# Optimization experiments

Measured on AMD Instinct MI355X. Metric: run time of the kernel, lower is better.

Reference implementation:

```python
import jax, jax.numpy as jnp
import numpy as np

B, S, D = 2, 2048, 1024
E, K = 8, 2
H = 1792  # round_up(int(1024*5/3)=1706, 256)


def setup_inputs() -> dict:
    key = jax.random.key(0)
    k1, k2, k3, k4, k5 = jax.random.split(key, 5)
    scale = 0.02
    x = jax.random.normal(k1, (B, S, D), dtype=jnp.float32)
    gate_w = jax.random.normal(k2, (E, D), dtype=jnp.float32) * scale   # nn.Linear(D,E).weight
    w_gate = jax.random.normal(k3, (E, D, H), dtype=jnp.float32) * scale
    w_up = jax.random.normal(k4, (E, D, H), dtype=jnp.float32) * scale
    w_down = jax.random.normal(k5, (E, H, D), dtype=jnp.float32) * scale
    return {"x": x, "gate_w": gate_w, "w_gate": w_gate, "w_up": w_up, "w_down": w_down}


def reference(x, gate_w, w_gate, w_up, w_down):
    b, s, d = x.shape
    x_flat = x.reshape(-1, d)                      # [T, D]
    # Gate computed in bf16 (torch autocast) then cast back to f32.
    logits = (x_flat.astype(jnp.bfloat16) @ gate_w.T.astype(jnp.bfloat16)).astype(jnp.float32)  # [T, E]
    topk_w, topk_idx = jax.lax.top_k(logits, K)    # [T, K]
    topk_w = jax.nn.softmax(topk_w, axis=-1)
    probs = jax.nn.softmax(logits, axis=-1)        # [T, E]
    mean_probs = probs.mean(0)                     # [E]
    load_balance_loss = E * jnp.sum(mean_probs ** 2)
    # Per-token combine weight for each expert (equivalent to sort/split/index_add combine).
    combine = jnp.sum(jax.nn.one_hot(topk_idx, E, dtype=x_flat.dtype) * topk_w[..., None], axis=1)  # [T, E]
    out = jnp.zeros_like(x_flat)
    for e in range(E):  # fixed small expert loop; math identical to grouped dispatch
        g = x_flat @ w_gate[e]                     # [T, H]
        u = x_flat @ w_up[e]                       # [T, H]
        y = (jax.nn.silu(g) * u) @ w_down[e]       # [T, D]
        out = out + y * combine[:, e:e + 1]
    return out.reshape(b, s, d), load_balance_loss, mean_probs
```

## Files before the change

kernel.cpp:

```cpp
#include <hip/hip_runtime.h>
#include <stdint.h>

#define TT 4096
#define DD 1024
#define EE 8
#define HH 1792
#define MP 10240
#define MT256 40
#define MT128 80

typedef __attribute__((ext_vector_type(8))) short short8;
typedef __attribute__((ext_vector_type(4))) short short4v;
typedef __attribute__((ext_vector_type(4))) float f32x4;

static __device__ __forceinline__ unsigned short f2bf(float f) {
  union { float f; uint32_t u; } v; v.f = f;
  return (unsigned short)((v.u + 0x7fffu + ((v.u >> 16) & 1u)) >> 16);
}
static __device__ __forceinline__ float bf2f(unsigned short h) {
  union { uint32_t u; float f; } v; v.u = ((uint32_t)h) << 16;
  return v.f;
}

static __device__ __forceinline__ void gll16(const void* g, const void* l) {
  __builtin_amdgcn_global_load_lds(
      (const __attribute__((address_space(1))) unsigned int*)g,
      (__attribute__((address_space(3))) unsigned int*)l, 16, 0, 0);
}

__global__ __launch_bounds__(256) void transpose_convert(
    const float* __restrict__ in, unsigned short* __restrict__ outp, int R, int C,
    int ilv, int sel) {
  __shared__ float t[64][68];
  const float* src = in + (size_t)blockIdx.z * R * C + (size_t)(blockIdx.x * 64) * C +
                     blockIdx.y * 64;
  unsigned short* dst = outp + (size_t)blockIdx.z * R * C * (ilv ? 2 : 1);
  const int tid = threadIdx.x;
  const int lr = tid >> 2, lc = (tid & 3) * 16;
#pragma unroll
  for (int q = 0; q < 4; ++q) {
    const f32x4 v = *(const f32x4*)(src + (size_t)lr * C + lc + 4 * q);
    t[lr][lc + 4 * q + 0] = v[0]; t[lr][lc + 4 * q + 1] = v[1];
    t[lr][lc + 4 * q + 2] = v[2]; t[lr][lc + 4 * q + 3] = v[3];
  }
  __syncthreads();
  unsigned short b[16];
#pragma unroll
  for (int q = 0; q < 16; ++q) b[q] = f2bf(t[lc + q][lr]);
  const int cg = blockIdx.y * 64 + lr;
  const int prow = ilv ? ((cg >> 4) * 32 + sel * 16 + (cg & 15)) : cg;
  unsigned short* d = dst + (size_t)prow * R + blockIdx.x * 64 + lc;
  *(short8*)(d) = *(const short8*)&b[0];
  *(short8*)(d + 8) = *(const short8*)&b[8];
}

__global__ __launch_bounds__(256) void gate_kernel(
    const float* __restrict__ x, const float* __restrict__ gw,
    float* __restrict__ combine, float* __restrict__ probs, int2* __restrict__ topk) {
  const int lane = threadIdx.x & 63;
  const int wave = threadIdx.x >> 6;
  const int t = blockIdx.x * 4 + wave;
  const float* xr = x + (size_t)t * DD;
  float acc[EE];
#pragma unroll
  for (int e = 0; e < EE; ++e) acc[e] = 0.f;
  for (int i = 0; i < DD / 64; ++i) {
    const int d = i * 64 + lane;
    const float xv = bf2f(f2bf(xr[d]));
#pragma unroll
    for (int e = 0; e < EE; ++e)
      acc[e] += xv * bf2f(f2bf(gw[e * DD + d]));
  }
#pragma unroll
  for (int e = 0; e < EE; ++e) {
#pragma unroll
    for (int off = 32; off > 0; off >>= 1)
      acc[e] += __shfl_xor(acc[e], off, 64);
  }
  if (lane == 0) {
    float lg[EE];
#pragma unroll
    for (int e = 0; e < EE; ++e) lg[e] = bf2f(f2bf(acc[e]));
    float m1 = -1e30f, m2 = -1e30f; int i1 = 0, i2 = 0;
#pragma unroll
    for (int e = 0; e < EE; ++e) {
      const float v = lg[e];
      if (v > m1) { m2 = m1; i2 = i1; m1 = v; i1 = e; }
      else if (v > m2) { m2 = v; i2 = e; }
    }
    const float e2 = expf(m2 - m1);
    const float w1 = 1.f / (1.f + e2);
    const float w2 = e2 * w1;
    float cb[EE];
#pragma unroll
    for (int e = 0; e < EE; ++e) cb[e] = 0.f;
    cb[i1] = w1; cb[i2] += w2;
    float p[EE]; float s = 0.f;
#pragma unroll
    for (int e = 0; e < EE; ++e) { p[e] = expf(lg[e] - m1); s += p[e]; }
    const float inv = 1.f / s;
#pragma unroll
    for (int e = 0; e < EE; ++e) {
      combine[(size_t)t * EE + e] = cb[e];
      probs[(size_t)t * EE + e] = p[e] * inv;
    }
    topk[t] = make_int2(i1, i2);
  }
}

__global__ __launch_bounds__(256) void reduce_kernel(
    const float* __restrict__ probs, float* __restrict__ tail) {
  const int tid = threadIdx.x;
  const int lane = tid & 63, wave = tid >> 6;
  float acc[EE];
#pragma unroll
  for (int e = 0; e < EE; ++e) acc[e] = 0.f;
  for (int t = tid; t < TT; t += 256) {
#pragma unroll
    for (int e = 0; e < EE; ++e) acc[e] += probs[(size_t)t * EE + e];
  }
#pragma unroll
  for (int e = 0; e < EE; ++e) {
#pragma unroll
    for (int off = 32; off > 0; off >>= 1)
      acc[e] += __shfl_xor(acc[e], off, 64);
  }
  __shared__ float sm[4][EE];
  if (lane == 0) {
#pragma unroll
    for (int e = 0; e < EE; ++e) sm[wave][e] = acc[e];
  }
  __syncthreads();
  if (tid == 0) {
    float loss = 0.f;
#pragma unroll
    for (int e = 0; e < EE; ++e) {
      const float m = (sm[0][e] + sm[1][e] + sm[2][e] + sm[3][e]) * (1.f / TT);
      tail[1 + e] = m;
      loss += m * m;
    }
    tail[0] = (float)EE * loss;
  }
}

__global__ __launch_bounds__(512) void route_kernel(
    const int2* __restrict__ topk, const float* __restrict__ combine,
    int* __restrict__ tok_list, float* __restrict__ wt_list,
    int* __restrict__ tab256, int* __restrict__ tab128) {
  const int lane = threadIdx.x & 63;
  const int e = threadIdx.x >> 6;
  __shared__ int cnts[EE], offs[EE];
  int cnt = 0;
  for (int i = 0; i < TT / 64; ++i) {
    const int2 k2 = topk[i * 64 + lane];
    cnt += __popcll(__ballot(k2.x == e || k2.y == e));
  }
  if (lane == 0) cnts[e] = cnt;
  __syncthreads();
  if (threadIdx.x == 0) {
    int off = 0, n256 = 0, n128 = 0;
    for (int f = 0; f < EE; ++f) {
      offs[f] = off;
      const int pc = (cnts[f] + 255) & ~255;
      for (int j = 0; j < (pc >> 8); ++j) {
        tab256[2 * n256] = f; tab256[2 * n256 + 1] = off + 256 * j; ++n256;
      }
      for (int j = 0; j < (pc >> 7); ++j) {
        tab128[2 * n128] = f; tab128[2 * n128 + 1] = off + 128 * j; ++n128;
      }
      off += pc;
    }
    for (; n256 < MT256; ++n256) { tab256[2 * n256] = -1; tab256[2 * n256 + 1] = 0; }
    for (; n128 < MT128; ++n128) { tab128[2 * n128] = -1; tab128[2 * n128 + 1] = 0; }
  }
  __syncthreads();
  int pos = offs[e];
  for (int i = 0; i < TT / 64; ++i) {
    const int t = i * 64 + lane;
    const int2 k2 = topk[t];
    const bool sel = (k2.x == e || k2.y == e);
    const unsigned long long m = __ballot(sel);
    if (sel) {
      const int p = pos + __popcll(m & ((1ull << lane) - 1ull));
      tok_list[p] = t;
      wt_list[p] = combine[(size_t)t * EE + e];
    }
    pos += __popcll(m);
  }
  const int pc = (cnt + 255) & ~255;
  for (int s = cnt + lane; s < pc; s += 64) {
    tok_list[offs[e] + s] = 0;
    wt_list[offs[e] + s] = 0.f;
  }
}

__global__ __launch_bounds__(256) void gather_x(
    const float* __restrict__ x, const int* __restrict__ tok_list,
    const int* __restrict__ tab256, unsigned short* __restrict__ xg) {
  const int e = tab256[2 * blockIdx.x];
  if (e < 0) return;
  const int row0 = tab256[2 * blockIdx.x + 1] + blockIdx.y * 16;
  const int tid = threadIdx.x;
#pragma unroll
  for (int i = 0; i < 16; ++i) {
    const int row = row0 + i;
    const int tok = tok_list[row];
    const f32x4 v = *(const f32x4*)(x + (size_t)tok * DD + tid * 4);
    unsigned short b[4] = {f2bf(v[0]), f2bf(v[1]), f2bf(v[2]), f2bf(v[3])};
    *(short4v*)(xg + (size_t)row * DD + tid * 4) = *(const short4v*)b;
  }
}

template <int MODE>
__global__ __launch_bounds__(256, 3) void gemm128(
    const unsigned short* __restrict__ Ab, const unsigned short* __restrict__ Bb,
    const int* __restrict__ tab, const int* __restrict__ tok_list,
    const float* __restrict__ wt_list, unsigned short* __restrict__ act,
    float* __restrict__ out) {
  constexpr int K   = (MODE == 0) ? DD : HH;
  constexpr int NBR = (MODE == 0) ? 2 * HH : DD;
  constexpr int NNT = NBR / 128;
  __shared__ unsigned short As[128 * 64];
  __shared__ unsigned short Bs[128 * 64];

  const int nwg = gridDim.x;
  const int wgid = (blockIdx.x & 7) * (nwg >> 3) + (blockIdx.x >> 3);
  const int mt = wgid / NNT, nt = wgid % NNT;
  const int e = tab[2 * mt];
  if (e < 0) return;
  const int row0 = tab[2 * mt + 1];
  const int n0 = nt * 128;

  const int tid = threadIdx.x, lane = tid & 63, wave = tid >> 6;
  const int wm = (wave >> 1) * 64, wn = (wave & 1) * 64;
  const int fr = lane & 15, hi = lane >> 4;

  const unsigned short* At = Ab + (size_t)row0 * K;
  const unsigned short* Bt = Bb + ((size_t)e * NBR + n0) * K;

  const int srel = tid * 16;
  const int srow0 = srel >> 7;
  const int sch = (srel >> 4) & 7;

  f32x4 acc[4][4];
#pragma unroll
  for (int i = 0; i < 4; ++i)
#pragma unroll
    for (int j = 0; j < 4; ++j) acc[i][j] = (f32x4){0.f, 0.f, 0.f, 0.f};

  for (int k0 = 0; k0 < K; k0 += 64) {
#pragma unroll
    for (int q = 0; q < 4; ++q) {
      const int row = q * 32 + srow0;
      gll16(At + (size_t)row * K + k0 + ((sch ^ (row & 7)) << 3),
            (const char*)As + q * 4096 + srel);
    }
#pragma unroll
    for (int q = 0; q < 4; ++q) {
      const int row = q * 32 + srow0;
      gll16(Bt + (size_t)row * K + k0 + ((sch ^ (row & 7)) << 3),
            (const char*)Bs + q * 4096 + srel);
    }
    __syncthreads();
#pragma unroll
    for (int kc = 0; kc < 2; ++kc) {
      short8 a[4], b[4];
#pragma unroll
      for (int i = 0; i < 4; ++i) {
        const int row = wm + i * 16 + fr;
        const int byt = (row * 128 + kc * 64 + hi * 16) ^ ((row & 7) << 4);
        a[i] = *(const short8*)((const char*)As + byt);
      }
#pragma unroll
      for (int j = 0; j < 4; ++j) {
        const int row = wn + j * 16 + fr;
        const int byt = (row * 128 + kc * 64 + hi * 16) ^ ((row & 7) << 4);
        b[j] = *(const short8*)((const char*)Bs + byt);
      }
#pragma unroll
      for (int i = 0; i < 4; ++i)
#pragma unroll
        for (int j = 0; j < 4; ++j)
          acc[i][j] = __builtin_amdgcn_mfma_f32_16x16x32_bf16(a[i], b[j], acc[i][j], 0, 0, 0);
    }
    __syncthreads();
  }

  const int r4 = hi * 4;
  if constexpr (MODE == 0) {
#pragma unroll
    for (int i = 0; i < 4; ++i)
#pragma unroll
      for (int r = 0; r < 4; ++r) {
        const int row = row0 + wm + i * 16 + r4 + r;
#pragma unroll
        for (int jj = 0; jj < 2; ++jj) {
          const float g = acc[i][2 * jj][r], u = acc[i][2 * jj + 1][r];
          const int nb = n0 + wn + jj * 32;
          const int h = ((nb >> 5) << 4) + fr;
          act[(size_t)row * HH + h] = f2bf((g / (1.f + expf(-g))) * u);
        }
      }
  } else {
#pragma unroll
    for (int i = 0; i < 4; ++i)
#pragma unroll
      for (int r = 0; r < 4; ++r) {
        const int rl = row0 + wm + i * 16 + r4 + r;
        const int tok = tok_list[rl];
        const float wt = wt_list[rl];
        if (wt != 0.f) {
#pragma unroll
          for (int j = 0; j < 4; ++j)
            unsafeAtomicAdd(&out[(size_t)tok * DD + n0 + wn + j * 16 + fr],
                            acc[i][j][r] * wt);
        }
      }
  }
}

extern "C" void kernel_launch(void* const* d_in, const int* in_sizes, int n_in,
                              void* d_out, int out_size, void* d_ws, size_t ws_size,
                              hipStream_t stream) {
  const float* x      = (const float*)d_in[0];
  const float* gw     = (const float*)d_in[1];
  const float* w_gate = (const float*)d_in[2];
  const float* w_up   = (const float*)d_in[3];
  const float* w_down = (const float*)d_in[4];
  float* out = (float*)d_out;
  float* tail = out + (size_t)TT * DD;

  char* w = (char*)d_ws;
  size_t o = 0;
  auto carve = [&](size_t bytes) { char* p = w + o; o += (bytes + 255) & ~255ull; return p; };
  unsigned short* wguT = (unsigned short*)carve((size_t)EE * 2 * HH * DD * 2);
  unsigned short* wdT  = (unsigned short*)carve((size_t)EE * DD * HH * 2);
  unsigned short* xg   = (unsigned short*)carve((size_t)MP * DD * 2);
  unsigned short* act  = (unsigned short*)carve((size_t)MP * HH * 2);
  float* combine = (float*)carve((size_t)TT * EE * 4);
  float* probs   = (float*)carve((size_t)TT * EE * 4);
  int2* topk     = (int2*)carve((size_t)TT * 8);
  int* tok_list  = (int*)carve((size_t)MP * 4);
  float* wt_list = (float*)carve((size_t)MP * 4);
  int* tab256    = (int*)carve((size_t)MT256 * 8);
  int* tab128    = (int*)carve((size_t)MT128 * 8);

  hipMemsetAsync(out, 0, (size_t)TT * DD * sizeof(float), stream);

  transpose_convert<<<dim3(DD / 64, HH / 64, EE), 256, 0, stream>>>(w_gate, wguT, DD, HH, 1, 0);
  transpose_convert<<<dim3(DD / 64, HH / 64, EE), 256, 0, stream>>>(w_up,   wguT, DD, HH, 1, 1);
  transpose_convert<<<dim3(HH / 64, DD / 64, EE), 256, 0, stream>>>(w_down, wdT,  HH, DD, 0, 0);

  gate_kernel<<<TT / 4, 256, 0, stream>>>(x, gw, combine, probs, topk);
  reduce_kernel<<<1, 256, 0, stream>>>(probs, tail);
  route_kernel<<<1, 512, 0, stream>>>(topk, combine, tok_list, wt_list, tab256, tab128);
  gather_x<<<dim3(MT256, 16), 256, 0, stream>>>(x, tok_list, tab256, xg);

  gemm128<0><<<MT128 * 28, 256, 0, stream>>>(xg, wguT, tab128, nullptr, nullptr, act, nullptr);
  gemm128<1><<<MT128 * 8, 256, 0, stream>>>(act, wdT, tab128, tok_list, wt_list, nullptr, out);
}
```

Baseline: 273.1 us.

## Replace gate/up GEMM with 256x256 double-buffered 8-wave pipelined kernel

```diff
diff --git a/kernel.cpp b/kernel.cpp
--- a/kernel.cpp
+++ b/kernel.cpp
@@ -211,15 +211,178 @@
   }
 }
 
-template <int MODE>
-__global__ __launch_bounds__(256, 3) void gemm128(
+#define MID_SYNC                                     \
+  __builtin_amdgcn_sched_barrier(0);                 \
+  __builtin_amdgcn_s_barrier();                      \
+  asm volatile("s_waitcnt lgkmcnt(0)" ::: "memory"); \
+  __builtin_amdgcn_sched_barrier(0);
+#define MID_SYNC_V4                                  \
+  __builtin_amdgcn_sched_barrier(0);                 \
+  asm volatile("s_waitcnt vmcnt(4)" ::: "memory");   \
+  __builtin_amdgcn_s_barrier();                      \
+  __builtin_amdgcn_sched_barrier(0);
+#define END_SYNC                                     \
+  __builtin_amdgcn_sched_barrier(0);                 \
+  __builtin_amdgcn_s_barrier();
+
+__global__ __launch_bounds__(512, 2) void gemm256(
+    const unsigned short* __restrict__ Ab, const unsigned short* __restrict__ Bb,
+    const int* __restrict__ tab, unsigned short* __restrict__ act) {
+  constexpr int K = DD;
+  constexpr int NK = K / 64;
+  constexpr int NNT = 14;
+  extern __shared__ char lds[];
+
+  const int nwg = gridDim.x;
+  const int wgid = (blockIdx.x & 7) * (nwg >> 3) + (blockIdx.x >> 3);
+  const int mt = wgid / NNT, nt = wgid % NNT;
+  const int e = tab[2 * mt];
+  if (e < 0) return;
+  const int row0 = tab[2 * mt + 1];
+  const int n0 = nt * 256;
+
+  const int tid = threadIdx.x, lane = tid & 63, wave = tid >> 6;
+  const int wm = (wave >> 2) * 128, wn = (wave & 3) * 64;
+  const int fr = lane & 15, hi = lane >> 4;
+
+  const unsigned short* At = Ab + (size_t)row0 * K;
+  const unsigned short* Bt = Bb + ((size_t)e * 2 * HH + n0) * K;
+
+  asm volatile("s_waitcnt vmcnt(0)" ::: "memory");
+
+  auto stage = [&](int u, int p, int h) {
+    const unsigned short* src = (h >= 2) ? Bt : At;
+    const int rbase = (h & 1) * 128;
+#pragma unroll
+    for (int q = 0; q < 2; ++q) {
+      const int rel = q * 8192 + tid * 16;
+      const int row = rel >> 7;
+      const int ch = (rel >> 4) & 7;
+      gll16(src + (size_t)(rbase + row) * K + u * 64 + ((ch ^ (row & 7)) << 3),
+            lds + p * 65536 + h * 16384 + rel);
+    }
+  };
+  auto rdA = [&](int p, int m, int kc) -> short8 {
+    const int lr = m & 127;
+    return *(const short8*)(lds + p * 65536 + ((m >> 7) << 14) + lr * 128 +
+                            ((((kc << 2) + hi) ^ (lr & 7)) << 4));
+  };
+  auto rdB = [&](int p, int n, int kc) -> short8 {
+    const int lr = n & 127;
+    return *(const short8*)(lds + p * 65536 + 32768 + ((n >> 7) << 14) + lr * 128 +
+                            ((((kc << 2) + hi) ^ (lr & 7)) << 4));
+  };
+
+  f32x4 acc[8][4];
+#pragma unroll
+  for (int i = 0; i < 8; ++i)
+#pragma unroll
+    for (int j = 0; j < 4; ++j) acc[i][j] = (f32x4){0.f, 0.f, 0.f, 0.f};
+  short8 a03[4][2], a47[4][2], b01[2][2], b23[2][2];
+
+  stage(0, 0, 2); stage(0, 0, 0); stage(0, 0, 3); stage(0, 0, 1);
+  stage(1, 1, 2); stage(1, 1, 0);
+  asm volatile("s_waitcnt vmcnt(4)" ::: "memory");
+  __builtin_amdgcn_s_barrier();
+
+  auto ktile = [&](int p, int un1, int pn1, int un2, int pn2) {
+#pragma unroll
+    for (int i = 0; i < 4; ++i)
+#pragma unroll
+      for (int kc = 0; kc < 2; ++kc) a03[i][kc] = rdA(p, wm + i * 16 + fr, kc);
+#pragma unroll
+    for (int j = 0; j < 2; ++j)
+#pragma unroll
+      for (int kc = 0; kc < 2; ++kc) b01[j][kc] = rdB(p, wn + j * 16 + fr, kc);
+    stage(un1, pn1, 3);
+    MID_SYNC
+    __builtin_amdgcn_s_setprio(1);
+#pragma unroll
+    for (int i = 0; i < 4; ++i)
+#pragma unroll
+      for (int j = 0; j < 2; ++j)
+#pragma unroll
+        for (int kc = 0; kc < 2; ++kc)
+          acc[i][j] = __builtin_amdgcn_mfma_f32_16x16x32_bf16(a03[i][kc], b01[j][kc], acc[i][j], 0, 0, 0);
+    __builtin_amdgcn_s_setprio(0);
+    END_SYNC
+#pragma unroll
+    for (int j = 0; j < 2; ++j)
+#pragma unroll
+      for (int kc = 0; kc < 2; ++kc) b23[j][kc] = rdB(p, wn + 32 + j * 16 + fr, kc);
+    stage(un1, pn1, 1);
+    MID_SYNC
+    __builtin_amdgcn_s_setprio(1);
+#pragma unroll
+    for (int i = 0; i < 4; ++i)
+#pragma unroll
+      for (int j = 0; j < 2; ++j)
+#pragma unroll
+        for (int kc = 0; kc < 2; ++kc)
+          acc[i][2 + j] = __builtin_amdgcn_mfma_f32_16x16x32_bf16(a03[i][kc], b23[j][kc], acc[i][2 + j], 0, 0, 0);
+    __builtin_amdgcn_s_setprio(0);
+    END_SYNC
+#pragma unroll
+    for (int i = 0; i < 4; ++i)
+#pragma unroll
+      for (int kc = 0; kc < 2; ++kc) a47[i][kc] = rdA(p, wm + 64 + i * 16 + fr, kc);
+    stage(un2, pn2, 2);
+    MID_SYNC
+    __builtin_amdgcn_s_setprio(1);
+#pragma unroll
+    for (int i = 0; i < 4; ++i)
+#pragma unroll
+      for (int j = 0; j < 2; ++j)
+#pragma unroll
+        for (int kc = 0; kc < 2; ++kc)
+          acc[4 + i][j] = __builtin_amdgcn_mfma_f32_16x16x32_bf16(a47[i][kc], b01[j][kc], acc[4 + i][j], 0, 0, 0);
+    __builtin_amdgcn_s_setprio(0);
+    END_SYNC
+    stage(un2, pn2, 0);
+    MID_SYNC_V4
+    __builtin_amdgcn_s_setprio(1);
+#pragma unroll
+    for (int i = 0; i < 4; ++i)
+#pragma unroll
+      for (int j = 0; j < 2; ++j)
+#pragma unroll
+        for (int kc = 0; kc < 2; ++kc)
+          acc[4 + i][2 + j] = __builtin_amdgcn_mfma_f32_16x16x32_bf16(a47[i][kc], b23[j][kc], acc[4 + i][2 + j], 0, 0, 0);
+    __builtin_amdgcn_s_setprio(0);
+    END_SYNC
+  };
+
+#pragma unroll 1
+  for (int tt = 0; tt < NK; tt += 2) {
+    const int u2 = (tt + 2 < NK) ? tt + 2 : tt;
+    const int u3 = (tt + 3 < NK) ? tt + 3 : tt + 1;
+    ktile(0, tt + 1, 1, u2, 0);
+    ktile(1, u2, 0, u3, 1);
+  }
+  asm volatile("s_waitcnt vmcnt(0)" ::: "memory");
+
+  const int r4 = hi * 4;
+#pragma unroll
+  for (int i = 0; i < 8; ++i)
+#pragma unroll
+    for (int r = 0; r < 4; ++r) {
+      const int row = row0 + wm + i * 16 + r4 + r;
+#pragma unroll
+      for (int jj = 0; jj < 2; ++jj) {
+        const float g = acc[i][2 * jj][r], u = acc[i][2 * jj + 1][r];
+        const int nb = n0 + wn + jj * 32;
+        const int h = ((nb >> 5) << 4) + fr;
+        act[(size_t)row * HH + h] = f2bf((g / (1.f + expf(-g))) * u);
+      }
+    }
+}
+
+__global__ __launch_bounds__(256, 3) void gemm128d(
     const unsigned short* __restrict__ Ab, const unsigned short* __restrict__ Bb,
     const int* __restrict__ tab, const int* __restrict__ tok_list,
-    const float* __restrict__ wt_list, unsigned short* __restrict__ act,
-    float* __restrict__ out) {
-  constexpr int K   = (MODE == 0) ? DD : HH;
-  constexpr int NBR = (MODE == 0) ? 2 * HH : DD;
-  constexpr int NNT = NBR / 128;
+    const float* __restrict__ wt_list, float* __restrict__ out) {
+  constexpr int K   = HH;
+  constexpr int NNT = 8;
   __shared__ unsigned short As[128 * 64];
   __shared__ unsigned short Bs[128 * 64];
 
@@ -236,7 +399,7 @@
   const int fr = lane & 15, hi = lane >> 4;
 
   const unsigned short* At = Ab + (size_t)row0 * K;
-  const unsigned short* Bt = Bb + ((size_t)e * NBR + n0) * K;
+  const unsigned short* Bt = Bb + ((size_t)e * DD + n0) * K;
 
   const int srel = tid * 16;
   const int srow0 = srel >> 7;
@@ -268,14 +431,12 @@
 #pragma unroll
       for (int i = 0; i < 4; ++i) {
         const int row = wm + i * 16 + fr;
-        const int byt = (row * 128 + kc * 64 + hi * 16) ^ ((row & 7) << 4);
-        a[i] = *(const short8*)((const char*)As + byt);
+        a[i] = *(const short8*)((const char*)As + ((row * 128 + kc * 64 + hi * 16) ^ ((row & 7) << 4)));
       }
 #pragma unroll
       for (int j = 0; j < 4; ++j) {
         const int row = wn + j * 16 + fr;
-        const int byt = (row * 128 + kc * 64 + hi * 16) ^ ((row & 7) << 4);
-        b[j] = *(const short8*)((const char*)Bs + byt);
+        b[j] = *(const short8*)((const char*)Bs + ((row * 128 + kc * 64 + hi * 16) ^ ((row & 7) << 4)));
       }
 #pragma unroll
       for (int i = 0; i < 4; ++i)
@@ -287,36 +448,20 @@
   }
 
   const int r4 = hi * 4;
-  if constexpr (MODE == 0) {
-#pragma unroll
-    for (int i = 0; i < 4; ++i)
-#pragma unroll
-      for (int r = 0; r < 4; ++r) {
-        const int row = row0 + wm + i * 16 + r4 + r;
-#pragma unroll
-        for (int jj = 0; jj < 2; ++jj) {
-          const float g = acc[i][2 * jj][r], u = acc[i][2 * jj + 1][r];
-          const int nb = n0 + wn + jj * 32;
-          const int h = ((nb >> 5) << 4) + fr;
-          act[(size_t)row * HH + h] = f2bf((g / (1.f + expf(-g))) * u);
-        }
+#pragma unroll
+  for (int i = 0; i < 4; ++i)
+#pragma unroll
+    for (int r = 0; r < 4; ++r) {
+      const int rl = row0 + wm + i * 16 + r4 + r;
+      const int tok = tok_list[rl];
+      const float wt = wt_list[rl];
+      if (wt != 0.f) {
+#pragma unroll
+        for (int j = 0; j < 4; ++j)
+          unsafeAtomicAdd(&out[(size_t)tok * DD + n0 + wn + j * 16 + fr],
+                          acc[i][j][r] * wt);
       }
-  } else {
-#pragma unroll
-    for (int i = 0; i < 4; ++i)
-#pragma unroll
-      for (int r = 0; r < 4; ++r) {
-        const int rl = row0 + wm + i * 16 + r4 + r;
-        const int tok = tok_list[rl];
-        const float wt = wt_list[rl];
-        if (wt != 0.f) {
-#pragma unroll
-          for (int j = 0; j < 4; ++j)
-            unsafeAtomicAdd(&out[(size_t)tok * DD + n0 + wn + j * 16 + fr],
-                            acc[i][j][r] * wt);
-        }
-      }
-  }
+    }
 }
 
 extern "C" void kernel_launch(void* const* d_in, const int* in_sizes, int n_in,
@@ -356,6 +501,8 @@
   route_kernel<<<1, 512, 0, stream>>>(topk, combine, tok_list, wt_list, tab256, tab128);
   gather_x<<<dim3(MT256, 16), 256, 0, stream>>>(x, tok_list, tab256, xg);
 
-  gemm128<0><<<MT128 * 28, 256, 0, stream>>>(xg, wguT, tab128, nullptr, nullptr, act, nullptr);
-  gemm128<1><<<MT128 * 8, 256, 0, stream>>>(act, wdT, tab128, tok_list, wt_list, nullptr, out);
-}
+  hipFuncSetAttribute(reinterpret_cast<const void*>(&gemm256),
+                      hipFuncAttributeMaxDynamicSharedMemorySize, 131072);
+  gemm256<<<MT256 * 14, 512, 131072, stream>>>(xg, wguT, tab256, act);
+  gemm128d<<<MT128 * 8, 256, 0, stream>>>(act, wdT, tab128, tok_list, wt_list, out);
+}
```

After: 289.0 us. +5.8%, slower.
